# Optimization experiments

Hardware: AMD Instinct MI355X
Metric: run time of the kernel (lower is better)

Reference implementation:

```python
import jax, jax.numpy as jnp
import numpy as np

N_NODES = 100000
N_EDGES = 1600000
DIMS = [128, 128, 40]   # embedding_dim
SS_DIM = 64
DROP_P = 0.2


def setup_inputs() -> dict:
    key = jax.random.key(0)
    ks = jax.random.split(key, 8)
    x = jax.random.normal(ks[0], (N_NODES, DIMS[0]), dtype=jnp.float32)
    adj_row = jax.random.randint(ks[1], (N_EDGES,), 0, N_NODES)
    adj_col = jax.random.randint(ks[2], (N_EDGES,), 0, N_NODES)
    adj_val = jax.random.uniform(ks[3], (N_EDGES,), dtype=jnp.float32)
    # nn.Linear(in, out, bias=False): y = x @ W.T; store transposed as (in, out)
    def lin(k, fi, fo):
        b = 1.0 / np.sqrt(fi)
        return jax.random.uniform(k, (fi, fo), minval=-b, maxval=b, dtype=jnp.float32)
    W0 = lin(ks[4], DIMS[0], DIMS[1])
    W1 = lin(ks[5], DIMS[1], DIMS[2])
    Wss = lin(ks[6], DIMS[-2], SS_DIM)
    return {"x": x, "adj_row": adj_row, "adj_col": adj_col, "adj_val": adj_val,
            "W0": W0, "W1": W1, "Wss": Wss}


def reference(x, adj_row, adj_col, adj_val, W0, W1, Wss):
    N = x.shape[0]
    keep = 1.0 - DROP_P

    def spmm(h):  # sparse [N,N] @ dense [N,d] via gather + segment_sum
        return jax.ops.segment_sum(adj_val[:, None] * h[adj_col], adj_row,
                                   num_segments=N)

    # deterministic dropout masks (fixed key, training path val_test=False)
    k1, k2 = jax.random.split(jax.random.key(42))
    m1 = jax.random.bernoulli(k1, keep, (N, W0.shape[1]))
    m2 = jax.random.bernoulli(k2, keep, (N, W0.shape[1]))

    # main branch: ln=0 -> spmm, lin0, relu, dropout; ln=1 -> spmm, lin1
    h = jnp.where(m1, jax.nn.relu(spmm(x) @ W0) / keep, 0.0)
    h = spmm(h) @ W1

    # self-supervised branch: ln=0 -> spmm, lin0, relu, dropout; ln=1 -> spmm; classifier
    s = jnp.where(m2, jax.nn.relu(spmm(x) @ W0) / keep, 0.0)
    s = spmm(s) @ Wss
    return (h, s)
```

## Files before the change

### kernel.cpp

```cpp
#include <hip/hip_runtime.h>
#include <stdint.h>


#define NN 100000
#define NE 1600000
#define D 128
#define NW 400000
#define ZC 104
#define DO1 40
#define DO2 64
#define OUT_S_OFF 4000000
#define KEEP_THR 6710886u
#define NB 49
#define CAP 36000
#define BINB 196
#define CONVB 12500
#define CSRB 49
#define MASKB1K 782

typedef unsigned int uint;
typedef __attribute__((ext_vector_type(4))) float f32x4;
typedef __attribute__((ext_vector_type(8))) short short8;
union U4S8 { uint4 u; short8 s; };

__device__ __forceinline__ float bflo(uint p) { return __uint_as_float(p << 16); }
__device__ __forceinline__ float bfhi(uint p) { return __uint_as_float(p & 0xffff0000u); }
__device__ __forceinline__ uint f2bf(float f) {
  uint u = __float_as_uint(f);
  return (u + 0x7fffu + ((u >> 16) & 1u)) >> 16;
}
__device__ __forceinline__ uint pack2(float lo, float hi) {
  return f2bf(lo) | (f2bf(hi) << 16);
}

__device__ __forceinline__ void tf2x32(uint k0, uint k1, uint x0, uint x1,
                                       uint& o0, uint& o1) {
  uint ks2 = k0 ^ k1 ^ 0x1BD11BDAu;
  x0 += k0; x1 += k1;
#define TFR(r) { x0 += x1; x1 = (x1 << (r)) | (x1 >> (32 - (r))); x1 ^= x0; }
  TFR(13) TFR(15) TFR(26) TFR(6)
  x0 += k1;  x1 += ks2 + 1u;
  TFR(17) TFR(29) TFR(16) TFR(24)
  x0 += ks2; x1 += k0 + 2u;
  TFR(13) TFR(15) TFR(26) TFR(6)
  x0 += k0;  x1 += k1 + 3u;
  TFR(17) TFR(29) TFR(16) TFR(24)
  x0 += k1;  x1 += ks2 + 4u;
  TFR(13) TFR(15) TFR(26) TFR(6)
  x0 += ks2; x1 += k0 + 5u;
#undef TFR
  o0 = x0; o1 = x1;
}

__global__ void bin_conv_kernel(const int* __restrict__ row, const int* __restrict__ col,
                                const float* __restrict__ val, int* __restrict__ cursor,
                                uint2* __restrict__ buck,
                                const float* __restrict__ x, uint* __restrict__ xb,
                                const float* __restrict__ W0, const float* __restrict__ W1,
                                const float* __restrict__ Wss,
                                ushort* __restrict__ w0t, ushort* __restrict__ wcatT) {
  int bid = blockIdx.x, tid = threadIdx.x;
  if (bid < BINB) {
    __shared__ int h[NB];
    __shared__ int base[NB];
    if (tid < NB) h[tid] = 0;
    __syncthreads();
    int e0 = bid * 8192;
#pragma unroll 4
    for (int j = 0; j < 32; ++j) {
      int e = e0 + j * 256 + tid;
      if (e < NE) atomicAdd(&h[row[e] >> 11], 1);
    }
    __syncthreads();
    if (tid < NB) {
      int c = h[tid];
      base[tid] = c ? (tid * CAP + atomicAdd(&cursor[tid], c)) : 0;
      h[tid] = 0;
    }
    __syncthreads();
#pragma unroll 4
    for (int j = 0; j < 32; ++j) {
      int e = e0 + j * 256 + tid;
      if (e < NE) {
        int r = row[e];
        int b = r >> 11;
        int k = atomicAdd(&h[b], 1);
        int idx = base[b] + k;
        int lim = (b + 1) * CAP;
        if (idx >= lim) idx = lim - 1;
        buck[idx] = make_uint2(((uint)(r & 2047) << 17) | (uint)col[e],
                               __float_as_uint(val[e]));
      }
    }
  } else if (bid < BINB + CONVB) {
    int i = (bid - BINB) * 256 + tid;
    float4 v = ((const float4*)x)[i];
    ((uint2*)xb)[i] = make_uint2(pack2(v.x, v.y), pack2(v.z, v.w));
  } else {
    int idx = (bid - BINB - CONVB) * 256 + tid;
    if (idx < 16384) {
      int c = idx >> 7, k = idx & 127;
      w0t[idx] = (ushort)f2bf(W0[k * D + c]);
    } else {
      int j = idx - 16384;
      int c = j >> 7, k = j & 127;
      float v = (c < 40) ? W1[k * DO1 + c] : ((c < 48) ? 0.f : Wss[k * DO2 + (c - 48)]);
      wcatT[j] = (ushort)f2bf(v);
    }
  }
}

__global__ __launch_bounds__(1024) void csr_mask_kernel(
    const uint2* __restrict__ buck, const int* __restrict__ cursor,
    int* __restrict__ ptr, uint2* __restrict__ cv,
    uint* __restrict__ m1, uint* __restrict__ m2) {
  int bid = blockIdx.x, tid = threadIdx.x;
  if (bid >= CSRB) {
    int t = (bid - CSRB) * 1024 + tid;
    if (t >= 2 * NW) return;
    uint a0, a1, b0, b1;
    tf2x32(0u, 42u, 0u, 0u, a0, a1);
    tf2x32(0u, 42u, 0u, 1u, b0, b1);
    bool second = (t >= NW);
    uint w  = second ? (uint)(t - NW) : (uint)t;
    uint k0 = second ? b0 : a0;
    uint k1 = second ? b1 : a1;
    uint base = w * 32u;
    uint word = 0u;
    for (int i = 0; i < 32; ++i) {
      uint o0, o1;
      tf2x32(k0, k1, 0u, base + (uint)i, o0, o1);
      word |= (uint)(((o0 ^ o1) >> 9) <= KEEP_THR) << i;
    }
    (second ? m2 : m1)[w] = word;
    return;
  }
  __shared__ int cnt[2048];
  __shared__ int sc[2048];
  __shared__ int cb[NB];
  int b = bid;
  if (tid < NB) cb[tid] = min(cursor[tid], CAP);
  int i0 = tid, i1 = tid + 1024;
  cnt[i0] = 0; cnt[i1] = 0;
  __syncthreads();
  int gbase = 0;
  for (int i = 0; i < b; ++i) gbase += cb[i];
  int n = cb[b];
  int src = b * CAP;
  for (int i = tid; i < n; i += 1024) atomicAdd(&cnt[buck[src + i].x >> 17], 1);
  __syncthreads();
  sc[i0] = cnt[i0]; sc[i1] = cnt[i1];
  __syncthreads();
  for (int off = 1; off < 2048; off <<= 1) {
    int v0 = (i0 >= off) ? sc[i0 - off] : 0;
    int v1 = (i1 >= off) ? sc[i1 - off] : 0;
    __syncthreads();
    sc[i0] += v0; sc[i1] += v1;
    __syncthreads();
  }
  int r0 = b * 2048;
  int s0 = sc[i0] - cnt[i0], s1 = sc[i1] - cnt[i1];
  if (r0 + i0 < NN) ptr[r0 + i0] = gbase + s0;
  if (r0 + i1 < NN) ptr[r0 + i1] = gbase + s1;
  if (b == 0 && tid == 0) ptr[NN] = NE;
  cnt[i0] = s0; cnt[i1] = s1;
  __syncthreads();
  for (int i = tid; i < n; i += 1024) {
    uint2 e = buck[src + i];
    int rl = e.x >> 17;
    int k = atomicAdd(&cnt[rl], 1);
    cv[gbase + k] = make_uint2(e.x & 0x1FFFFu, e.y);
  }
}

__global__ void spmm_x_kernel(const int* __restrict__ ptr, const uint2* __restrict__ cv,
                              const uint2* __restrict__ xb, uint2* __restrict__ t) {
  int r = blockIdx.x * 8 + (threadIdx.x >> 5);
  int k = threadIdx.x & 31;
  int s = ptr[r], e = ptr[r + 1];
  float a0 = 0.f, a1 = 0.f, a2 = 0.f, a3 = 0.f;
  int i = s;
  for (; i + 4 <= e; i += 4) {
    uint2 e0 = cv[i], e1 = cv[i + 1], e2 = cv[i + 2], e3 = cv[i + 3];
    uint2 p0 = xb[e0.x * 32 + k];
    uint2 p1 = xb[e1.x * 32 + k];
    uint2 p2 = xb[e2.x * 32 + k];
    uint2 p3 = xb[e3.x * 32 + k];
    float v0 = __uint_as_float(e0.y), v1 = __uint_as_float(e1.y);
    float v2 = __uint_as_float(e2.y), v3 = __uint_as_float(e3.y);
    a0 += v0 * bflo(p0.x); a1 += v0 * bfhi(p0.x);
    a2 += v0 * bflo(p0.y); a3 += v0 * bfhi(p0.y);
    a0 += v1 * bflo(p1.x); a1 += v1 * bfhi(p1.x);
    a2 += v1 * bflo(p1.y); a3 += v1 * bfhi(p1.y);
    a0 += v2 * bflo(p2.x); a1 += v2 * bfhi(p2.x);
    a2 += v2 * bflo(p2.y); a3 += v2 * bfhi(p2.y);
    a0 += v3 * bflo(p3.x); a1 += v3 * bfhi(p3.x);
    a2 += v3 * bflo(p3.y); a3 += v3 * bfhi(p3.y);
  }
  for (; i < e; ++i) {
    uint2 ev = cv[i];
    float v = __uint_as_float(ev.y);
    uint2 p = xb[ev.x * 32 + k];
    a0 += v * bflo(p.x); a1 += v * bfhi(p.x);
    a2 += v * bflo(p.y); a3 += v * bfhi(p.y);
  }
  t[r * 32 + k] = make_uint2(pack2(a0, a1), pack2(a2, a3));
}

#define SWZ(row, byte) ((row) * 256 + ((byte) ^ ((((row) >> 1) & 7) << 4)))
__global__ __launch_bounds__(512, 4) void pass_a_kernel(
    const uint* __restrict__ tb, const ushort* __restrict__ w0t,
    const ushort* __restrict__ wcatT,
    const uint* __restrict__ m1, const uint* __restrict__ m2,
    ushort* __restrict__ zz) {
  __shared__ __align__(16) char ldsb[69632];
  uint* mlds = (uint*)(ldsb + 65536);

  int t = threadIdx.x;
  int r0 = blockIdx.x * 128;
  int wid = t >> 6, l = t & 63, lc = l & 15, lk = l >> 4;

#pragma unroll
  for (int i = 0; i < 4; ++i) {
    int lin = i * 512 + t;
    int row = lin >> 4, seg = lin & 15;
    int gr = r0 + row;
    uint4 v = make_uint4(0, 0, 0, 0);
    if (gr < NN) v = ((const uint4*)(tb + (size_t)gr * 64))[seg];
    *(uint4*)&ldsb[SWZ(row, seg * 16)] = v;
    uint4 w = ((const uint4*)w0t)[lin];
    *(uint4*)&ldsb[32768 + SWZ(row, seg * 16)] = w;
  }
#pragma unroll
  for (int i = 0; i < 2; ++i) {
    int idx = t;
    int row = idx >> 2, word = idx & 3;
    int gr = r0 + row;
    uint v = 0;
    if (gr < NN) v = (i == 0 ? m1 : m2)[gr * 4 + word];
    mlds[i * 512 + idx] = v;
  }
  __syncthreads();

  short8 af[4];
#pragma unroll
  for (int s = 0; s < 4; ++s) {
    U4S8 tmp; tmp.u = *(uint4*)&ldsb[SWZ(16 * wid + lc, 64 * s + 16 * lk)];
    af[s] = tmp.s;
  }
  f32x4 acc[8];
#pragma unroll
  for (int n = 0; n < 8; ++n) acc[n] = (f32x4)(0.f);
#pragma unroll
  for (int n = 0; n < 8; ++n) {
#pragma unroll
    for (int s = 0; s < 4; ++s) {
      U4S8 tmp; tmp.u = *(uint4*)&ldsb[32768 + SWZ(16 * n + lc, 64 * s + 16 * lk)];
      acc[n] = __builtin_amdgcn_mfma_f32_16x16x32_bf16(af[s], tmp.s, acc[n], 0, 0, 0);
    }
  }
  __syncthreads();

#pragma unroll
  for (int reg = 0; reg < 4; ++reg) {
    int row = 16 * wid + 4 * lk + reg;
    uint4 w1q = *(uint4*)&mlds[row * 4];
    uint4 w2q = *(uint4*)&mlds[512 + row * 4];
    uint w1a[4] = {w1q.x, w1q.y, w1q.z, w1q.w};
    uint w2a[4] = {w2q.x, w2q.y, w2q.z, w2q.w};
#pragma unroll
    for (int n = 0; n < 8; ++n) {
      float v = fmaxf(acc[n][reg], 0.f) * 1.25f;
      ushort ub = (ushort)f2bf(v);
      int bit = (n & 1) * 16 + lc;
      ushort u1 = ((w1a[n >> 1] >> bit) & 1u) ? ub : (ushort)0;
      ushort u2 = ((w2a[n >> 1] >> bit) & 1u) ? ub : (ushort)0;
      int ad = SWZ(row, 32 * n + 2 * lc);
      *(ushort*)&ldsb[ad] = u1;
      *(ushort*)&ldsb[32768 + ad] = u2;
    }
  }
  __syncthreads();

  f32x4 acc2[7];
#pragma unroll
  for (int n = 0; n < 7; ++n) acc2[n] = (f32x4)(0.f);
#pragma unroll
  for (int n2 = 0; n2 < 7; ++n2) {
    int ubase = (n2 < 3) ? 0 : 32768;
#pragma unroll
    for (int s = 0; s < 4; ++s) {
      U4S8 a2; a2.u = ((const uint4*)wcatT)[(16 * n2 + lc) * 16 + 4 * s + lk];
      U4S8 b2; b2.u = *(uint4*)&ldsb[ubase + SWZ(16 * wid + lc, 64 * s + 16 * lk)];
      acc2[n2] = __builtin_amdgcn_mfma_f32_16x16x32_bf16(a2.s, b2.s, acc2[n2], 0, 0, 0);
    }
  }

  int r = r0 + 16 * wid + lc;
  if (r < NN) {
#pragma unroll
    for (int n2 = 0; n2 < 7; ++n2) {
      if (n2 == 2 && lk >= 2) continue;
      int cb = 16 * n2 + 4 * lk;
      if (n2 >= 3) cb -= 8;
      uint2 v = make_uint2(pack2(acc2[n2][0], acc2[n2][1]),
                           pack2(acc2[n2][2], acc2[n2][3]));
      *(uint2*)(zz + (size_t)r * ZC + cb) = v;
    }
  }
}

__global__ void gather_out_kernel(const int* __restrict__ ptr, const uint2* __restrict__ cv,
                                  const uint2* __restrict__ zp, float* __restrict__ out) {
  int r = blockIdx.x * 8 + (threadIdx.x >> 5);
  int k = threadIdx.x & 31;
  if (k >= 26) return;
  int s = ptr[r], e = ptr[r + 1];
  float a0 = 0.f, a1 = 0.f, a2 = 0.f, a3 = 0.f;
  int i = s;
  for (; i + 4 <= e; i += 4) {
    uint2 e0 = cv[i], e1 = cv[i + 1], e2 = cv[i + 2], e3 = cv[i + 3];
    uint2 p0 = zp[e0.x * 26 + k];
    uint2 p1 = zp[e1.x * 26 + k];
    uint2 p2 = zp[e2.x * 26 + k];
    uint2 p3 = zp[e3.x * 26 + k];
    float v0 = __uint_as_float(e0.y), v1 = __uint_as_float(e1.y);
    float v2 = __uint_as_float(e2.y), v3 = __uint_as_float(e3.y);
    a0 += v0 * bflo(p0.x); a1 += v0 * bfhi(p0.x);
    a2 += v0 * bflo(p0.y); a3 += v0 * bfhi(p0.y);
    a0 += v1 * bflo(p1.x); a1 += v1 * bfhi(p1.x);
    a2 += v1 * bflo(p1.y); a3 += v1 * bfhi(p1.y);
    a0 += v2 * bflo(p2.x); a1 += v2 * bfhi(p2.x);
    a2 += v2 * bflo(p2.y); a3 += v2 * bfhi(p2.y);
    a0 += v3 * bflo(p3.x); a1 += v3 * bfhi(p3.x);
    a2 += v3 * bflo(p3.y); a3 += v3 * bfhi(p3.y);
  }
  for (; i < e; ++i) {
    uint2 ev = cv[i];
    float v = __uint_as_float(ev.y);
    uint2 p = zp[ev.x * 26 + k];
    a0 += v * bflo(p.x); a1 += v * bfhi(p.x);
    a2 += v * bflo(p.y); a3 += v * bfhi(p.y);
  }
  if (k < 10) {
    *(float4*)(out + (size_t)r * DO1 + 4 * k) = make_float4(a0, a1, a2, a3);
  } else {
    *(float4*)(out + OUT_S_OFF + (size_t)r * DO2 + 4 * (k - 10)) = make_float4(a0, a1, a2, a3);
  }
}

extern "C" void kernel_launch(void* const* d_in, const int* in_sizes, int n_in,
                              void* d_out, int out_size, void* d_ws, size_t ws_size,
                              hipStream_t stream) {
  const float* x       = (const float*)d_in[0];
  const int*   adj_row = (const int*)d_in[1];
  const int*   adj_col = (const int*)d_in[2];
  const float* adj_val = (const float*)d_in[3];
  const float* W0      = (const float*)d_in[4];
  const float* W1      = (const float*)d_in[5];
  const float* Wss     = (const float*)d_in[6];
  float* out = (float*)d_out;

  char* ws = (char*)d_ws;
  uint*   t_bf  = (uint*)(ws + 0);
  uint2*  buck  = (uint2*)(ws + 0);
  uint*   xb    = (uint*)(ws + 25600000);
  ushort* zz    = (ushort*)(ws + 25600000);
  uint*   m1    = (uint*)(ws + 51200000);
  uint*   m2    = (uint*)(ws + 52800000);
  int*    ptr   = (int*)(ws + 54400000);
  ushort* w0t   = (ushort*)(ws + 54800016);
  ushort* wcatT = (ushort*)(ws + 54832784);
  int*    curs  = (int*)(ws + 54861456);
  uint2*  cv    = (uint2*)(ws + 55600016);

  hipMemsetAsync(curs, 0, NB * sizeof(int), stream);
  bin_conv_kernel<<<BINB + CONVB + 120, 256, 0, stream>>>(
      adj_row, adj_col, adj_val, curs, buck, x, xb, W0, W1, Wss, w0t, wcatT);
  csr_mask_kernel<<<CSRB + MASKB1K, 1024, 0, stream>>>(buck, curs, ptr, cv, m1, m2);
  spmm_x_kernel<<<12500, 256, 0, stream>>>(ptr, cv, (const uint2*)xb, (uint2*)t_bf);
  pass_a_kernel<<<782, 512, 0, stream>>>(t_bf, w0t, wcatT, m1, m2, zz);
  gather_out_kernel<<<12500, 256, 0, stream>>>(ptr, cv, (const uint2*)zz, out);
}
```

Before: 282.7 us.

## Rebalance prep kernels pairing mask with binning and x-conversion with CSR; unroll gathers by 8

The dropout-mask generation now shares a launch with edge binning, and the x-to-bf16 conversion shares a launch with the CSR build. This evens out compute-heavy and memory-heavy work across the two prep kernels so each launch overlaps dissimilar work. Both SpMM gather loops are unrolled to 8 edges so more independent loads are in flight per wave, which raises register use. The mask blocks drop the old bounds check, which only holds because 3125*256 exactly equals 2*NW.

```diff
diff --git a/kernel.cpp b/kernel.cpp
--- a/kernel.cpp
+++ b/kernel.cpp
@@ -14,9 +14,9 @@
 #define NB 49
 #define CAP 36000
 #define BINB 196
-#define CONVB 12500
+#define MASKB 3125
 #define CSRB 49
-#define MASKB1K 782
+#define CONV1K 3125
 
 typedef unsigned int uint;
 typedef __attribute__((ext_vector_type(4))) float f32x4;
@@ -52,13 +52,13 @@
   o0 = x0; o1 = x1;
 }
 
-__global__ void bin_conv_kernel(const int* __restrict__ row, const int* __restrict__ col,
-                                const float* __restrict__ val, int* __restrict__ cursor,
-                                uint2* __restrict__ buck,
-                                const float* __restrict__ x, uint* __restrict__ xb,
-                                const float* __restrict__ W0, const float* __restrict__ W1,
-                                const float* __restrict__ Wss,
-                                ushort* __restrict__ w0t, ushort* __restrict__ wcatT) {
+__global__ void bin_mask_prep_kernel(const int* __restrict__ row, const int* __restrict__ col,
+                                     const float* __restrict__ val, int* __restrict__ cursor,
+                                     uint2* __restrict__ buck,
+                                     uint* __restrict__ m1, uint* __restrict__ m2,
+                                     const float* __restrict__ W0, const float* __restrict__ W1,
+                                     const float* __restrict__ Wss,
+                                     ushort* __restrict__ w0t, ushort* __restrict__ wcatT) {
   int bid = blockIdx.x, tid = threadIdx.x;
   if (bid < BINB) {
     __shared__ int h[NB];
@@ -92,32 +92,8 @@
                                __float_as_uint(val[e]));
       }
     }
-  } else if (bid < BINB + CONVB) {
-    int i = (bid - BINB) * 256 + tid;
-    float4 v = ((const float4*)x)[i];
-    ((uint2*)xb)[i] = make_uint2(pack2(v.x, v.y), pack2(v.z, v.w));
-  } else {
-    int idx = (bid - BINB - CONVB) * 256 + tid;
-    if (idx < 16384) {
-      int c = idx >> 7, k = idx & 127;
-      w0t[idx] = (ushort)f2bf(W0[k * D + c]);
-    } else {
-      int j = idx - 16384;
-      int c = j >> 7, k = j & 127;
-      float v = (c < 40) ? W1[k * DO1 + c] : ((c < 48) ? 0.f : Wss[k * DO2 + (c - 48)]);
-      wcatT[j] = (ushort)f2bf(v);
-    }
-  }
-}
-
-__global__ __launch_bounds__(1024) void csr_mask_kernel(
-    const uint2* __restrict__ buck, const int* __restrict__ cursor,
-    int* __restrict__ ptr, uint2* __restrict__ cv,
-    uint* __restrict__ m1, uint* __restrict__ m2) {
-  int bid = blockIdx.x, tid = threadIdx.x;
-  if (bid >= CSRB) {
-    int t = (bid - CSRB) * 1024 + tid;
-    if (t >= 2 * NW) return;
+  } else if (bid < BINB + MASKB) {
+    int t = (bid - BINB) * 256 + tid;
     uint a0, a1, b0, b1;
     tf2x32(0u, 42u, 0u, 0u, a0, a1);
     tf2x32(0u, 42u, 0u, 1u, b0, b1);
@@ -133,6 +109,29 @@
       word |= (uint)(((o0 ^ o1) >> 9) <= KEEP_THR) << i;
     }
     (second ? m2 : m1)[w] = word;
+  } else {
+    int idx = (bid - BINB - MASKB) * 256 + tid;
+    if (idx < 16384) {
+      int c = idx >> 7, k = idx & 127;
+      w0t[idx] = (ushort)f2bf(W0[k * D + c]);
+    } else {
+      int j = idx - 16384;
+      int c = j >> 7, k = j & 127;
+      float v = (c < 40) ? W1[k * DO1 + c] : ((c < 48) ? 0.f : Wss[k * DO2 + (c - 48)]);
+      wcatT[j] = (ushort)f2bf(v);
+    }
+  }
+}
+
+__global__ __launch_bounds__(1024) void csr_conv_kernel(
+    const uint2* __restrict__ buck, const int* __restrict__ cursor,
+    int* __restrict__ ptr, uint2* __restrict__ cv,
+    const float* __restrict__ x, uint* __restrict__ xb) {
+  int bid = blockIdx.x, tid = threadIdx.x;
+  if (bid >= CSRB) {
+    int i = (bid - CSRB) * 1024 + tid;
+    float4 v = ((const float4*)x)[i];
+    ((uint2*)xb)[i] = make_uint2(pack2(v.x, v.y), pack2(v.z, v.w));
     return;
   }
   __shared__ int cnt[2048];
@@ -180,22 +179,32 @@
   int s = ptr[r], e = ptr[r + 1];
   float a0 = 0.f, a1 = 0.f, a2 = 0.f, a3 = 0.f;
   int i = s;
-  for (; i + 4 <= e; i += 4) {
-    uint2 e0 = cv[i], e1 = cv[i + 1], e2 = cv[i + 2], e3 = cv[i + 3];
-    uint2 p0 = xb[e0.x * 32 + k];
-    uint2 p1 = xb[e1.x * 32 + k];
-    uint2 p2 = xb[e2.x * 32 + k];
-    uint2 p3 = xb[e3.x * 32 + k];
-    float v0 = __uint_as_float(e0.y), v1 = __uint_as_float(e1.y);
-    float v2 = __uint_as_float(e2.y), v3 = __uint_as_float(e3.y);
-    a0 += v0 * bflo(p0.x); a1 += v0 * bfhi(p0.x);
-    a2 += v0 * bflo(p0.y); a3 += v0 * bfhi(p0.y);
-    a0 += v1 * bflo(p1.x); a1 += v1 * bfhi(p1.x);
-    a2 += v1 * bflo(p1.y); a3 += v1 * bfhi(p1.y);
-    a0 += v2 * bflo(p2.x); a1 += v2 * bfhi(p2.x);
-    a2 += v2 * bflo(p2.y); a3 += v2 * bfhi(p2.y);
-    a0 += v3 * bflo(p3.x); a1 += v3 * bfhi(p3.x);
-    a2 += v3 * bflo(p3.y); a3 += v3 * bfhi(p3.y);
+  for (; i + 8 <= e; i += 8) {
+    uint2 ee[8], pp[8];
+#pragma unroll
+    for (int j = 0; j < 8; ++j) ee[j] = cv[i + j];
+#pragma unroll
+    for (int j = 0; j < 8; ++j) pp[j] = xb[ee[j].x * 32 + k];
+#pragma unroll
+    for (int j = 0; j < 8; ++j) {
+      float v = __uint_as_float(ee[j].y);
+      a0 += v * bflo(pp[j].x); a1 += v * bfhi(pp[j].x);
+      a2 += v * bflo(pp[j].y); a3 += v * bfhi(pp[j].y);
+    }
+  }
+  if (i + 4 <= e) {
+    uint2 ee[4], pp[4];
+#pragma unroll
+    for (int j = 0; j < 4; ++j) ee[j] = cv[i + j];
+#pragma unroll
+    for (int j = 0; j < 4; ++j) pp[j] = xb[ee[j].x * 32 + k];
+#pragma unroll
+    for (int j = 0; j < 4; ++j) {
+      float v = __uint_as_float(ee[j].y);
+      a0 += v * bflo(pp[j].x); a1 += v * bfhi(pp[j].x);
+      a2 += v * bflo(pp[j].y); a3 += v * bfhi(pp[j].y);
+    }
+    i += 4;
   }
   for (; i < e; ++i) {
     uint2 ev = cv[i];
@@ -318,22 +327,32 @@
   int s = ptr[r], e = ptr[r + 1];
   float a0 = 0.f, a1 = 0.f, a2 = 0.f, a3 = 0.f;
   int i = s;
-  for (; i + 4 <= e; i += 4) {
-    uint2 e0 = cv[i], e1 = cv[i + 1], e2 = cv[i + 2], e3 = cv[i + 3];
-    uint2 p0 = zp[e0.x * 26 + k];
-    uint2 p1 = zp[e1.x * 26 + k];
-    uint2 p2 = zp[e2.x * 26 + k];
-    uint2 p3 = zp[e3.x * 26 + k];
-    float v0 = __uint_as_float(e0.y), v1 = __uint_as_float(e1.y);
-    float v2 = __uint_as_float(e2.y), v3 = __uint_as_float(e3.y);
-    a0 += v0 * bflo(p0.x); a1 += v0 * bfhi(p0.x);
-    a2 += v0 * bflo(p0.y); a3 += v0 * bfhi(p0.y);
-    a0 += v1 * bflo(p1.x); a1 += v1 * bfhi(p1.x);
-    a2 += v1 * bflo(p1.y); a3 += v1 * bfhi(p1.y);
-    a0 += v2 * bflo(p2.x); a1 += v2 * bfhi(p2.x);
-    a2 += v2 * bflo(p2.y); a3 += v2 * bfhi(p2.y);
-    a0 += v3 * bflo(p3.x); a1 += v3 * bfhi(p3.x);
-    a2 += v3 * bflo(p3.y); a3 += v3 * bfhi(p3.y);
+  for (; i + 8 <= e; i += 8) {
+    uint2 ee[8], pp[8];
+#pragma unroll
+    for (int j = 0; j < 8; ++j) ee[j] = cv[i + j];
+#pragma unroll
+    for (int j = 0; j < 8; ++j) pp[j] = zp[ee[j].x * 26 + k];
+#pragma unroll
+    for (int j = 0; j < 8; ++j) {
+      float v = __uint_as_float(ee[j].y);
+      a0 += v * bflo(pp[j].x); a1 += v * bfhi(pp[j].x);
+      a2 += v * bflo(pp[j].y); a3 += v * bfhi(pp[j].y);
+    }
+  }
+  if (i + 4 <= e) {
+    uint2 ee[4], pp[4];
+#pragma unroll
+    for (int j = 0; j < 4; ++j) ee[j] = cv[i + j];
+#pragma unroll
+    for (int j = 0; j < 4; ++j) pp[j] = zp[ee[j].x * 26 + k];
+#pragma unroll
+    for (int j = 0; j < 4; ++j) {
+      float v = __uint_as_float(ee[j].y);
+      a0 += v * bflo(pp[j].x); a1 += v * bfhi(pp[j].x);
+      a2 += v * bflo(pp[j].y); a3 += v * bfhi(pp[j].y);
+    }
+    i += 4;
   }
   for (; i < e; ++i) {
     uint2 ev = cv[i];
@@ -375,9 +394,9 @@
   uint2*  cv    = (uint2*)(ws + 55600016);
 
   hipMemsetAsync(curs, 0, NB * sizeof(int), stream);
-  bin_conv_kernel<<<BINB + CONVB + 120, 256, 0, stream>>>(
-      adj_row, adj_col, adj_val, curs, buck, x, xb, W0, W1, Wss, w0t, wcatT);
-  csr_mask_kernel<<<CSRB + MASKB1K, 1024, 0, stream>>>(buck, curs, ptr, cv, m1, m2);
+  bin_mask_prep_kernel<<<BINB + MASKB + 120, 256, 0, stream>>>(
+      adj_row, adj_col, adj_val, curs, buck, m1, m2, W0, W1, Wss, w0t, wcatT);
+  csr_conv_kernel<<<CSRB + CONV1K, 1024, 0, stream>>>(buck, curs, ptr, cv, x, xb);
   spmm_x_kernel<<<12500, 256, 0, stream>>>(ptr, cv, (const uint2*)xb, (uint2*)t_bf);
   pass_a_kernel<<<782, 512, 0, stream>>>(t_bf, w0t, wcatT, m1, m2, zz);
   gather_out_kernel<<<12500, 256, 0, stream>>>(ptr, cv, (const uint2*)zz, out);
```

New measurement: 283.1 us. About the same (+0.1%).
